# Kernel optimization log

Measured on AMD Instinct MI355X. Metric: run time of the kernel, lower is better.

Reference implementation:

```python
import jax, jax.numpy as jnp
import numpy as np

N_NODES = 20000
N_EDGES = 320000
IN_CH = 512
HID = 128
HEADS = 4
OUT_CH = 30
NEG_SLOPE = 0.2  # PyG GATConv default negative_slope


def add_self_loops(ei, n):
    loops = jnp.arange(n, dtype=ei.dtype)
    return jnp.concatenate([ei, jnp.stack([loops, loops])], axis=1)


def gat_layer(x, ei, W, a_src, a_dst, b, concat):
    # x: [N, F_in], ei: [2, E] (source row 0 -> target row 1), W: [F_in, H*C]
    n = x.shape[0]
    H, C = a_src.shape
    h = (x @ W).reshape(n, H, C)                      # [N, H, C]
    src, dst = ei[0], ei[1]
    al_src = jnp.einsum('nhc,hc->nh', h, a_src)       # [N, H]
    al_dst = jnp.einsum('nhc,hc->nh', h, a_dst)
    e = al_src[src] + al_dst[dst]                     # [E, H]
    e = jnp.where(e > 0, e, NEG_SLOPE * e)            # LeakyReLU
    # segment softmax over destination nodes (stable)
    emax = jax.lax.stop_gradient(jax.ops.segment_max(e, dst, num_segments=n))
    p = jnp.exp(e - emax[dst])
    denom = jax.ops.segment_sum(p, dst, num_segments=n)
    alpha = p / denom[dst]                            # [E, H]
    msg = h[src] * alpha[:, :, None]                  # [E, H, C]
    out = jax.ops.segment_sum(msg, dst, num_segments=n)  # [N, H, C]
    out = out.reshape(n, H * C) if concat else out.mean(axis=1)
    return out + b


def setup_inputs() -> dict:
    key = jax.random.key(0)
    ks = jax.random.split(key, 12)
    s = 0.05
    x = jax.random.normal(ks[0], (N_NODES, IN_CH), jnp.float32)
    edge_index = jax.random.randint(ks[1], (2, N_EDGES), 0, N_NODES, jnp.int32)
    return {
        'x': x,
        'edge_index': edge_index,
        'W1': jax.random.normal(ks[2], (IN_CH, HEADS * HID), jnp.float32) * s,
        'a_src1': jax.random.normal(ks[3], (HEADS, HID), jnp.float32) * s,
        'a_dst1': jax.random.normal(ks[4], (HEADS, HID), jnp.float32) * s,
        'b1': jnp.zeros((HEADS * HID,), jnp.float32),
        'W2': jax.random.normal(ks[5], (HEADS * HID, OUT_CH), jnp.float32) * s,
        'a_src2': jax.random.normal(ks[6], (1, OUT_CH), jnp.float32) * s,
        'a_dst2': jax.random.normal(ks[7], (1, OUT_CH), jnp.float32) * s,
        'b2': jnp.zeros((OUT_CH,), jnp.float32),
        'Wd': jax.random.normal(ks[8], (OUT_CH, IN_CH), jnp.float32) * s,
        'bd': jnp.zeros((IN_CH,), jnp.float32),
    }


def reference(x, edge_index, W1, a_src1, a_dst1, b1, W2, a_src2, a_dst2, b2, Wd, bd):
    n = x.shape[0]
    ei = add_self_loops(edge_index, n)
    h = gat_layer(x, ei, W1, a_src1, a_dst1, b1, concat=True)   # [N, HEADS*HID]
    h = jax.nn.elu(h)                                           # dropout is identity in eval
    z = gat_layer(h, ei, W2, a_src2, a_dst2, b2, concat=False)  # [N, OUT_CH]
    x_hat = z @ Wd + bd                                         # [N, IN_CH]
    return (x_hat, z)
```

## Files before the change

kernel.cpp:

```cpp
#include <hip/hip_runtime.h>
#include <hip/hip_bf16.h>
#include <stdint.h>

#define N_NODES 20000
#define N_EDGES 320000
#define IN_CH 512
#define HID 128
#define HEADS 4
#define HC 512
#define OUT_CH 30
#define NEG_SLOPE 0.2f
#define M_PAD 20096
#define CAST_BLOCKS (M_PAD * IN_CH / 4 / 256)
#define G1_BLOCKS (M_PAD / 128 * 4)
#define EDGE_BLOCKS (N_EDGES / 256)
#define MAXDEG 64

typedef _Float16 half8 __attribute__((ext_vector_type(8)));
typedef _Float16 half4v __attribute__((ext_vector_type(4)));
typedef float f32x4 __attribute__((ext_vector_type(4)));

static __device__ __forceinline__ float lrelu(float e) { return e > 0.f ? e : NEG_SLOPE * e; }

static __device__ __forceinline__ void gload16(const void* gsrc, void* ldst) {
  __builtin_amdgcn_global_load_lds(
      (const __attribute__((address_space(1))) uint32_t*)gsrc,
      (__attribute__((address_space(3))) uint32_t*)ldst,
      16, 0, 0);
}

__global__ __launch_bounds__(256) void k_front(const float* __restrict__ x,
                                               const float* __restrict__ W1,
                                               const float* __restrict__ W2,
                                               _Float16* __restrict__ xh,
                                               _Float16* __restrict__ W1t,
                                               _Float16* __restrict__ w2t,
                                               int* __restrict__ cnt) {
  __shared__ float t[64][65];
  const int b = blockIdx.x;
  const int tid = threadIdx.x;
  if (b < CAST_BLOCKS) {
    int i = b * 256 + tid;
    if (i < N_NODES) cnt[i] = 0;
    int base = i * 4;
    int row = base >> 9;
    half4v o;
    if (row < N_NODES) {
      float4 v = *(const float4*)(x + (size_t)base);
      o[0] = (_Float16)v.x; o[1] = (_Float16)v.y; o[2] = (_Float16)v.z; o[3] = (_Float16)v.w;
    } else {
      o[0] = o[1] = o[2] = o[3] = (_Float16)0.f;
    }
    *(half4v*)(xh + (size_t)base) = o;
  } else if (b < CAST_BLOCKS + 64) {
    const int bb = b - CAST_BLOCKS;
    const int bk = (bb & 7) * 64;
    const int bn = (bb >> 3) * 64;
#pragma unroll
    for (int it = 0; it < 16; it++) {
      int idx = tid + it * 256;
      int r = idx >> 6, c = idx & 63;
      t[r][c] = W1[(size_t)(bk + r) * HC + bn + c];
    }
    __syncthreads();
#pragma unroll
    for (int it = 0; it < 16; it++) {
      int idx = tid + it * 256;
      int rn = idx >> 6, ck = idx & 63;
      W1t[(size_t)(bn + rn) * IN_CH + bk + ck] = (_Float16)t[ck][rn];
    }
  } else {
    int idx = (b - CAST_BLOCKS - 64) * 256 + tid;
    int n = idx >> 9, k = idx & 511;
    w2t[idx] = (n < OUT_CH) ? (_Float16)W2[(size_t)k * OUT_CH + n] : (_Float16)0.f;
  }
}

__global__ __launch_bounds__(256) void k_scatter(const int* __restrict__ src,
                                                 const int* __restrict__ dst,
                                                 int* __restrict__ cnt,
                                                 int* __restrict__ srcs) {
  int e = blockIdx.x * 256 + threadIdx.x;
  int d = dst[e];
  int pos = atomicAdd(&cnt[d], 1);
  if (pos < MAXDEG) srcs[(d << 6) + pos] = src[e];
}

__global__ __launch_bounds__(256) void k_gemm1_mfma(const _Float16* __restrict__ A,
                                                    const _Float16* __restrict__ Bt,
                                                    _Float16* __restrict__ C,
                                                    const float* __restrict__ a_src,
                                                    const float* __restrict__ a_dst,
                                                    float* __restrict__ al_s,
                                                    float* __restrict__ al_d) {
  __shared__ _Float16 smem[128 * 136];
  const int bx = blockIdx.x;
  const int tid = threadIdx.x;
  _Float16* As = smem;
  _Float16* Bs = smem + 128 * 64;
  _Float16* Cs = smem;
  const int lane = tid & 63;
  const int w = tid >> 6;
  const int bm = (bx >> 2) * 128;
  const int head = bx & 3;
  const int bn = head * 128;

  const int lrow = lane >> 3;
  const int schunk = (lane & 7) ^ lrow;

  const int wm = w >> 1, wn = w & 1;
  const int r15 = lane & 15;
  const int q = lane >> 4;
  const int a_row0 = wm * 64 + r15;
  const int b_row0 = wn * 64 + r15;

  f32x4 acc[4][4];
  const f32x4 zero = {0.f, 0.f, 0.f, 0.f};
#pragma unroll
  for (int i = 0; i < 4; i++)
#pragma unroll
    for (int j = 0; j < 4; j++) acc[i][j] = zero;

  for (int kb = 0; kb < 8; kb++) {
    const int kof = kb * 64 + schunk * 8;
#pragma unroll
    for (int t = 0; t < 4; t++) {
      const int row = w * 32 + t * 8;
      gload16(A + (size_t)(bm + row + lrow) * IN_CH + kof, (void*)(As + row * 64));
      gload16(Bt + (size_t)(bn + row + lrow) * IN_CH + kof, (void*)(Bs + row * 64));
    }
    __syncthreads();
#pragma unroll
    for (int s = 0; s < 2; s++) {
      const int cs = ((s * 4 + q) ^ (lane & 7)) * 8;
      half8 af[4], bf[4];
#pragma unroll
      for (int i = 0; i < 4; i++) af[i] = *(const half8*)&As[(a_row0 + i * 16) * 64 + cs];
#pragma unroll
      for (int j = 0; j < 4; j++) bf[j] = *(const half8*)&Bs[(b_row0 + j * 16) * 64 + cs];
#pragma unroll
      for (int i = 0; i < 4; i++)
#pragma unroll
        for (int j = 0; j < 4; j++)
          acc[i][j] = __builtin_amdgcn_mfma_f32_16x16x32_f16(af[i], bf[j], acc[i][j], 0, 0, 0);
    }
    __syncthreads();
  }
#pragma unroll
  for (int i = 0; i < 4; i++)
#pragma unroll
    for (int j = 0; j < 4; j++)
#pragma unroll
      for (int r = 0; r < 4; r++) {
        const int row = wm * 64 + i * 16 + q * 4 + r;
        const int col = wn * 64 + j * 16 + r15;
        Cs[row * 136 + col] = (_Float16)acc[i][j][r];
      }
  __syncthreads();
#pragma unroll
  for (int it = 0; it < 8; it++) {
    int cidx = tid + it * 256;
    int row = cidx >> 4, c16 = cidx & 15;
    int gm = bm + row;
    if (gm < N_NODES)
      *(half8*)(C + (size_t)gm * HC + bn + c16 * 8) = *(const half8*)&Cs[row * 136 + c16 * 8];
  }
  const int row = tid >> 1;
  const int hf = tid & 1;
  const float* asp = a_src + head * HID + hf * 64;
  const float* adp = a_dst + head * HID + hf * 64;
  float s = 0.f, d = 0.f;
#pragma unroll
  for (int j8 = 0; j8 < 8; j8++) {
    half8 cv = *(const half8*)&Cs[row * 136 + hf * 64 + j8 * 8];
    float4 a0 = *(const float4*)(asp + j8 * 8);
    float4 a1 = *(const float4*)(asp + j8 * 8 + 4);
    float4 d0 = *(const float4*)(adp + j8 * 8);
    float4 d1 = *(const float4*)(adp + j8 * 8 + 4);
    float c0 = (float)cv[0], c1 = (float)cv[1], c2 = (float)cv[2], c3 = (float)cv[3];
    float c4 = (float)cv[4], c5 = (float)cv[5], c6 = (float)cv[6], c7 = (float)cv[7];
    s += c0 * a0.x + c1 * a0.y + c2 * a0.z + c3 * a0.w +
         c4 * a1.x + c5 * a1.y + c6 * a1.z + c7 * a1.w;
    d += c0 * d0.x + c1 * d0.y + c2 * d0.z + c3 * d0.w +
         c4 * d1.x + c5 * d1.y + c6 * d1.z + c7 * d1.w;
  }
  s += __shfl_xor(s, 1);
  d += __shfl_xor(d, 1);
  const int gm = bm + row;
  if (hf == 0 && gm < N_NODES) {
    al_s[gm * HEADS + head] = s;
    al_d[gm * HEADS + head] = d;
  }
}

__global__ __launch_bounds__(256) void k_agg1(const _Float16* __restrict__ h,
                                              const float* __restrict__ al_s,
                                              const float* __restrict__ al_d,
                                              const int* __restrict__ cnta,
                                              const int* __restrict__ srcs,
                                              const float* __restrict__ b1,
                                              _Float16* __restrict__ hm) {
  __shared__ __align__(16) int2 s_sp[4][64];
  const int tid = threadIdx.x;
  const int lane = tid & 63;
  const int wv = tid >> 6;
  const int qq = lane >> 4;
  const int l16 = lane & 15;
  const int head = blockIdx.x / 1250;
  const int n = (blockIdx.x % 1250) * 16 + wv * 4 + qq;
  const int cb = head * HID + l16 * 8;

  const float adn = al_d[n * HEADS + head];
  const float pself = __expf(lrelu(al_s[n * HEADS + head] + adn));

  half8 hv = *(const half8*)(h + (size_t)n * HC + cb);
  float acc[8];
  float den = pself;
#pragma unroll
  for (int j = 0; j < 8; j++) acc[j] = pself * (float)hv[j];

  const int beg = n << 6;
  const int cnt = min(cnta[n], MAXDEG);
  int mx = cnt;
  mx = max(mx, __shfl_xor(mx, 16));
  mx = max(mx, __shfl_xor(mx, 32));

  for (int base = 0; base < mx; base += 16) {
    int sreg = n;
    float preg = 0.f;
    if (base + l16 < cnt) {
      sreg = srcs[beg + base + l16];
      preg = __expf(lrelu(al_s[sreg * HEADS + head] + adn));
    }
    s_sp[wv][lane] = make_int2(sreg, __float_as_int(preg));
    __builtin_amdgcn_wave_barrier();
    const int rem = cnt - base;
    const int m4 = rem > 16 ? 16 : ((rem + 3) & ~3);
    for (int k = 0; k < m4; k += 4) {
      int4 w0 = *(const int4*)&s_sp[wv][qq * 16 + k];
      int4 w1 = *(const int4*)&s_sp[wv][qq * 16 + k + 2];
      half8 v0 = *(const half8*)(h + (size_t)w0.x * HC + cb);
      half8 v1 = *(const half8*)(h + (size_t)w0.z * HC + cb);
      half8 v2 = *(const half8*)(h + (size_t)w1.x * HC + cb);
      half8 v3 = *(const half8*)(h + (size_t)w1.z * HC + cb);
      float p0 = __int_as_float(w0.y), p1 = __int_as_float(w0.w);
      float p2 = __int_as_float(w1.y), p3 = __int_as_float(w1.w);
      den += p0 + p1 + p2 + p3;
#pragma unroll
      for (int j = 0; j < 8; j++)
        acc[j] += p0 * (float)v0[j] + p1 * (float)v1[j] +
                  p2 * (float)v2[j] + p3 * (float)v3[j];
    }
    __builtin_amdgcn_wave_barrier();
  }
  const float inv = 1.f / den;
  float4 bb0 = *(const float4*)(b1 + cb);
  float4 bb1 = *(const float4*)(b1 + cb + 4);
  float ob[8] = {bb0.x, bb0.y, bb0.z, bb0.w, bb1.x, bb1.y, bb1.z, bb1.w};
  half8 ov;
#pragma unroll
  for (int j = 0; j < 8; j++) {
    float o = acc[j] * inv + ob[j];
    o = o > 0.f ? o : __expf(o) - 1.f;
    ov[j] = (_Float16)o;
  }
  *(half8*)(hm + (size_t)n * HC + cb) = ov;
}

__global__ __launch_bounds__(256) void k_gemm2_mfma(const _Float16* __restrict__ hm,
                                                    const _Float16* __restrict__ w2t,
                                                    const float* __restrict__ a_s2,
                                                    const float* __restrict__ a_d2,
                                                    float* __restrict__ zpre,
                                                    float* __restrict__ al_s2,
                                                    float* __restrict__ al_d2) {
  __shared__ _Float16 Bs[32 * 520];
  __shared__ _Float16 As[64 * 136];
  const int tid = threadIdx.x;
  const int lane = tid & 63;
  const int w = tid >> 6;
  const int bm = blockIdx.x * 64;
  const int n15 = lane & 15;
  const int q = lane >> 4;

#pragma unroll
  for (int it = 0; it < 8; it++) {
    int idx = (tid + it * 256) * 8;
    int n = idx >> 9, k = idx & 511;
    *(half8*)&Bs[n * 520 + k] = *(const half8*)(w2t + idx);
  }

  f32x4 acc0 = {0.f, 0.f, 0.f, 0.f}, acc1 = {0.f, 0.f, 0.f, 0.f};
  for (int kt = 0; kt < HC; kt += 128) {
#pragma unroll
    for (int p = 0; p < 4; p++) {
      int row = (tid >> 4) + p * 16;
      int kof = (tid & 15) * 8;
      int gm = bm + row;
      half8 v = {};
      if (gm < N_NODES) v = *(const half8*)(hm + (size_t)gm * HC + kt + kof);
      *(half8*)&As[row * 136 + kof] = v;
    }
    __syncthreads();
#pragma unroll
    for (int ks = 0; ks < 128; ks += 32) {
      half8 af = *(const half8*)&As[(w * 16 + n15) * 136 + ks + q * 8];
      half8 b0 = *(const half8*)&Bs[n15 * 520 + kt + ks + q * 8];
      half8 b1 = *(const half8*)&Bs[(16 + n15) * 520 + kt + ks + q * 8];
      acc0 = __builtin_amdgcn_mfma_f32_16x16x32_f16(af, b0, acc0, 0, 0, 0);
      acc1 = __builtin_amdgcn_mfma_f32_16x16x32_f16(af, b1, acc1, 0, 0, 0);
    }
    __syncthreads();
  }
  const float asn0 = (n15 < OUT_CH) ? a_s2[n15] : 0.f;
  const float asn1 = (n15 + 16 < OUT_CH) ? a_s2[n15 + 16] : 0.f;
  const float adn0 = (n15 < OUT_CH) ? a_d2[n15] : 0.f;
  const float adn1 = (n15 + 16 < OUT_CH) ? a_d2[n15 + 16] : 0.f;
#pragma unroll
  for (int r = 0; r < 4; r++) {
    const int gm = bm + w * 16 + q * 4 + r;
    const bool ok = gm < N_NODES;
    if (ok) {
      zpre[(size_t)gm * OUT_CH + n15] = acc0[r];
      if (n15 + 16 < OUT_CH) zpre[(size_t)gm * OUT_CH + n15 + 16] = acc1[r];
    }
    float s = acc0[r] * asn0 + acc1[r] * asn1;
    float d = acc0[r] * adn0 + acc1[r] * adn1;
#pragma unroll
    for (int off = 8; off; off >>= 1) {
      s += __shfl_xor(s, off);
      d += __shfl_xor(d, off);
    }
    if (n15 == 0 && ok) {
      al_s2[gm] = s;
      al_d2[gm] = d;
    }
  }
}

__global__ __launch_bounds__(256) void k_agg2dec(const float* __restrict__ zpre,
                                                 const float* __restrict__ al_s2,
                                                 const float* __restrict__ al_d2,
                                                 const int* __restrict__ cnta,
                                                 const int* __restrict__ srcs,
                                                 const float* __restrict__ b2,
                                                 const float* __restrict__ Wd,
                                                 const float* __restrict__ bd,
                                                 float* __restrict__ zout,
                                                 float* __restrict__ xhat) {
  __shared__ __align__(16) int2 s_sp[4][64];
  __shared__ float zs[8][32];
  const int tid = threadIdx.x;
  const int lane = tid & 63;
  const int wv = tid >> 6;
  const int hh = lane >> 5;
  const int l32 = lane & 31;
  const int n = blockIdx.x * 8 + wv * 2 + hh;
  const float ad2n = al_d2[n];
  const float pself = __expf(lrelu(al_s2[n] + ad2n));
  const bool act = l32 < OUT_CH;
  float zv = act ? zpre[(size_t)n * OUT_CH + l32] : 0.f;
  float acc = pself * zv;
  float den = pself;

  const int beg = n << 6;
  const int cnt = min(cnta[n], MAXDEG);
  int mx = max(cnt, __shfl_xor(cnt, 32));

  for (int base = 0; base < mx; base += 32) {
    int sreg = n;
    float preg = 0.f;
    if (base + l32 < cnt) {
      sreg = srcs[beg + base + l32];
      preg = __expf(lrelu(al_s2[sreg] + ad2n));
    }
    s_sp[wv][lane] = make_int2(sreg, __float_as_int(preg));
    __builtin_amdgcn_wave_barrier();
    const int rem = cnt - base;
    const int m4 = rem > 32 ? 32 : ((rem + 3) & ~3);
    for (int k = 0; k < m4; k += 4) {
      int4 w0 = *(const int4*)&s_sp[wv][hh * 32 + k];
      int4 w1 = *(const int4*)&s_sp[wv][hh * 32 + k + 2];
      float v0 = act ? zpre[(size_t)w0.x * OUT_CH + l32] : 0.f;
      float v1 = act ? zpre[(size_t)w0.z * OUT_CH + l32] : 0.f;
      float v2 = act ? zpre[(size_t)w1.x * OUT_CH + l32] : 0.f;
      float v3 = act ? zpre[(size_t)w1.z * OUT_CH + l32] : 0.f;
      float p0 = __int_as_float(w0.y), p1 = __int_as_float(w0.w);
      float p2 = __int_as_float(w1.y), p3 = __int_as_float(w1.w);
      den += p0 + p1 + p2 + p3;
      acc += p0 * v0 + p1 * v1 + p2 * v2 + p3 * v3;
    }
    __builtin_amdgcn_wave_barrier();
  }
  float zfin = 0.f;
  if (act) zfin = acc / den + b2[l32];
  zs[wv * 2 + hh][l32] = zfin;
  if (act) zout[(size_t)n * OUT_CH + l32] = zfin;
  __syncthreads();
  const int n0 = blockIdx.x * 8;
#pragma unroll
  for (int cc = 0; cc < 2; cc++) {
    const int c = cc * 256 + tid;
    float wd[32];
#pragma unroll
    for (int k = 0; k < OUT_CH; k++) wd[k] = Wd[(size_t)k * IN_CH + c];
    wd[30] = wd[31] = 0.f;
    const float b0 = bd[c];
#pragma unroll
    for (int i = 0; i < 8; i++) {
      float a0 = b0;
#pragma unroll
      for (int k4 = 0; k4 < 8; k4++) {
        float4 z4 = *(const float4*)&zs[i][k4 * 4];
        a0 += z4.x * wd[k4 * 4 + 0] + z4.y * wd[k4 * 4 + 1] +
              z4.z * wd[k4 * 4 + 2] + z4.w * wd[k4 * 4 + 3];
      }
      xhat[(size_t)(n0 + i) * IN_CH + c] = a0;
    }
  }
}

extern "C" void kernel_launch(void* const* d_in, const int* in_sizes, int n_in,
                              void* d_out, int out_size, void* d_ws, size_t ws_size,
                              hipStream_t stream) {
  const float* x    = (const float*)d_in[0];
  const int*   ei   = (const int*)d_in[1];
  const float* W1   = (const float*)d_in[2];
  const float* a_s1 = (const float*)d_in[3];
  const float* a_d1 = (const float*)d_in[4];
  const float* b1   = (const float*)d_in[5];
  const float* W2   = (const float*)d_in[6];
  const float* a_s2 = (const float*)d_in[7];
  const float* a_d2 = (const float*)d_in[8];
  const float* b2   = (const float*)d_in[9];
  const float* Wd   = (const float*)d_in[10];
  const float* bd   = (const float*)d_in[11];

  float* xhat = (float*)d_out;
  float* zout = xhat + (size_t)N_NODES * IN_CH;

  const int* srcv = ei;
  const int* dstv = ei + N_EDGES;

  char* w = (char*)d_ws;
  auto alloc = [&](size_t bytes) {
    void* p = (void*)w;
    w += (bytes + 255) & ~(size_t)255;
    return p;
  };
  _Float16* xh   = (_Float16*)alloc((size_t)M_PAD * IN_CH * 2);
  _Float16* w1t  = (_Float16*)alloc((size_t)HC * IN_CH * 2);
  _Float16* w2t  = (_Float16*)alloc((size_t)32 * HC * 2);
  _Float16* h    = (_Float16*)alloc((size_t)N_NODES * HC * 2);
  _Float16* hm   = (_Float16*)alloc((size_t)N_NODES * HC * 2);
  float* zpre  = (float*)alloc((size_t)N_NODES * OUT_CH * 4);
  float* al_s1v= (float*)alloc((size_t)N_NODES * HEADS * 4);
  float* al_d1v= (float*)alloc((size_t)N_NODES * HEADS * 4);
  float* al_s2v= (float*)alloc((size_t)N_NODES * 4);
  float* al_d2v= (float*)alloc((size_t)N_NODES * 4);
  int*   cnt   = (int*)alloc((size_t)N_NODES * 4);
  int*   srcs  = (int*)alloc((size_t)N_NODES * MAXDEG * 4);

  k_front<<<CAST_BLOCKS + 128, 256, 0, stream>>>(x, W1, W2, xh, w1t, w2t, cnt);
  k_scatter<<<EDGE_BLOCKS, 256, 0, stream>>>(srcv, dstv, cnt, srcs);
  k_gemm1_mfma<<<G1_BLOCKS, 256, 0, stream>>>(xh, w1t, h, a_s1, a_d1, al_s1v, al_d1v);
  k_agg1<<<1250 * HEADS, 256, 0, stream>>>(h, al_s1v, al_d1v, cnt, srcs, b1, hm);
  k_gemm2_mfma<<<(N_NODES + 63) / 64, 256, 0, stream>>>(hm, w2t, a_s2, a_d2, zpre,
                                                        al_s2v, al_d2v);
  k_agg2dec<<<N_NODES / 8, 256, 0, stream>>>(zpre, al_s2v, al_d2v, cnt, srcs, b2,
                                             Wd, bd, zout, xhat);
}
```

Measured before the change: 249.1 us.

## Fold edge scatter into front kernel and split aggregation from decoder GEMM

The edge-bucketing scatter now runs inside the front kernel alongside the casts and weight transposes, so one launch is gone. The count array is cleared by a memset beforehand instead of inside the kernel. The fused layer-2 aggregation and decoder is split into two kernels. The new decoder tile covers 64 nodes per block, which reuses the Wd registers across more rows. The trade-off is an extra launch plus a memset, and the z round-trip through global memory.

```diff
diff --git a/kernel.cpp b/kernel.cpp
--- a/kernel.cpp
+++ b/kernel.cpp
@@ -35,13 +35,23 @@
                                                _Float16* __restrict__ xh,
                                                _Float16* __restrict__ W1t,
                                                _Float16* __restrict__ w2t,
-                                               int* __restrict__ cnt) {
+                                               const int* __restrict__ src,
+                                               const int* __restrict__ dst,
+                                               int* __restrict__ cnt,
+                                               int* __restrict__ srcs) {
   __shared__ float t[64][65];
-  const int b = blockIdx.x;
-  const int tid = threadIdx.x;
+  const int b0 = blockIdx.x;
+  const int tid = threadIdx.x;
+  if (b0 < EDGE_BLOCKS) {
+    int e = b0 * 256 + tid;
+    int d = dst[e];
+    int pos = atomicAdd(&cnt[d], 1);
+    if (pos < MAXDEG) srcs[(d << 6) + pos] = src[e];
+    return;
+  }
+  const int b = b0 - EDGE_BLOCKS;
   if (b < CAST_BLOCKS) {
     int i = b * 256 + tid;
-    if (i < N_NODES) cnt[i] = 0;
     int base = i * 4;
     int row = base >> 9;
     half4v o;
@@ -74,16 +84,6 @@
     int n = idx >> 9, k = idx & 511;
     w2t[idx] = (n < OUT_CH) ? (_Float16)W2[(size_t)k * OUT_CH + n] : (_Float16)0.f;
   }
-}
-
-__global__ __launch_bounds__(256) void k_scatter(const int* __restrict__ src,
-                                                 const int* __restrict__ dst,
-                                                 int* __restrict__ cnt,
-                                                 int* __restrict__ srcs) {
-  int e = blockIdx.x * 256 + threadIdx.x;
-  int d = dst[e];
-  int pos = atomicAdd(&cnt[d], 1);
-  if (pos < MAXDEG) srcs[(d << 6) + pos] = src[e];
 }
 
 __global__ __launch_bounds__(256) void k_gemm1_mfma(const _Float16* __restrict__ A,
@@ -338,18 +338,14 @@
   }
 }
 
-__global__ __launch_bounds__(256) void k_agg2dec(const float* __restrict__ zpre,
-                                                 const float* __restrict__ al_s2,
-                                                 const float* __restrict__ al_d2,
-                                                 const int* __restrict__ cnta,
-                                                 const int* __restrict__ srcs,
-                                                 const float* __restrict__ b2,
-                                                 const float* __restrict__ Wd,
-                                                 const float* __restrict__ bd,
-                                                 float* __restrict__ zout,
-                                                 float* __restrict__ xhat) {
+__global__ __launch_bounds__(256) void k_agg2(const float* __restrict__ zpre,
+                                              const float* __restrict__ al_s2,
+                                              const float* __restrict__ al_d2,
+                                              const int* __restrict__ cnta,
+                                              const int* __restrict__ srcs,
+                                              const float* __restrict__ b2,
+                                              float* __restrict__ zout) {
   __shared__ __align__(16) int2 s_sp[4][64];
-  __shared__ float zs[8][32];
   const int tid = threadIdx.x;
   const int lane = tid & 63;
   const int wv = tid >> 6;
@@ -392,31 +388,39 @@
     }
     __builtin_amdgcn_wave_barrier();
   }
-  float zfin = 0.f;
-  if (act) zfin = acc / den + b2[l32];
-  zs[wv * 2 + hh][l32] = zfin;
-  if (act) zout[(size_t)n * OUT_CH + l32] = zfin;
+  if (act) zout[(size_t)n * OUT_CH + l32] = acc / den + b2[l32];
+}
+
+__global__ __launch_bounds__(256) void k_dec(const float* __restrict__ z,
+                                             const float* __restrict__ Wd,
+                                             const float* __restrict__ bd,
+                                             float* __restrict__ xhat) {
+  __shared__ float zs[64][32];
+  const int tid = threadIdx.x;
+  const int c = blockIdx.y * 256 + tid;
+  float wd[32];
+#pragma unroll
+  for (int k = 0; k < OUT_CH; k++) wd[k] = Wd[(size_t)k * IN_CH + c];
+  wd[30] = wd[31] = 0.f;
+  const int n0 = blockIdx.x * 64;
+  for (int idx = tid; idx < 64 * 32; idx += 256) {
+    int r = idx >> 5, cc = idx & 31;
+    int row = n0 + r;
+    zs[r][cc] = (cc < OUT_CH && row < N_NODES) ? z[(size_t)row * OUT_CH + cc] : 0.f;
+  }
   __syncthreads();
-  const int n0 = blockIdx.x * 8;
-#pragma unroll
-  for (int cc = 0; cc < 2; cc++) {
-    const int c = cc * 256 + tid;
-    float wd[32];
-#pragma unroll
-    for (int k = 0; k < OUT_CH; k++) wd[k] = Wd[(size_t)k * IN_CH + c];
-    wd[30] = wd[31] = 0.f;
-    const float b0 = bd[c];
-#pragma unroll
-    for (int i = 0; i < 8; i++) {
-      float a0 = b0;
-#pragma unroll
-      for (int k4 = 0; k4 < 8; k4++) {
-        float4 z4 = *(const float4*)&zs[i][k4 * 4];
-        a0 += z4.x * wd[k4 * 4 + 0] + z4.y * wd[k4 * 4 + 1] +
-              z4.z * wd[k4 * 4 + 2] + z4.w * wd[k4 * 4 + 3];
-      }
-      xhat[(size_t)(n0 + i) * IN_CH + c] = a0;
-    }
+  const float b0 = bd[c];
+  for (int i = 0; i < 64; i++) {
+    int row = n0 + i;
+    if (row >= N_NODES) break;
+    float a0 = b0;
+#pragma unroll
+    for (int k4 = 0; k4 < 8; k4++) {
+      float4 zv = *(const float4*)&zs[i][k4 * 4];
+      a0 += zv.x * wd[k4 * 4 + 0] + zv.y * wd[k4 * 4 + 1] +
+            zv.z * wd[k4 * 4 + 2] + zv.w * wd[k4 * 4 + 3];
+    }
+    xhat[(size_t)row * IN_CH + c] = a0;
   }
 }
 
@@ -461,12 +465,13 @@
   int*   cnt   = (int*)alloc((size_t)N_NODES * 4);
   int*   srcs  = (int*)alloc((size_t)N_NODES * MAXDEG * 4);
 
-  k_front<<<CAST_BLOCKS + 128, 256, 0, stream>>>(x, W1, W2, xh, w1t, w2t, cnt);
-  k_scatter<<<EDGE_BLOCKS, 256, 0, stream>>>(srcv, dstv, cnt, srcs);
+  hipMemsetAsync(cnt, 0, (size_t)N_NODES * 4, stream);
+  k_front<<<EDGE_BLOCKS + CAST_BLOCKS + 128, 256, 0, stream>>>(x, W1, W2, xh, w1t, w2t,
+                                                               srcv, dstv, cnt, srcs);
   k_gemm1_mfma<<<G1_BLOCKS, 256, 0, stream>>>(xh, w1t, h, a_s1, a_d1, al_s1v, al_d1v);
   k_agg1<<<1250 * HEADS, 256, 0, stream>>>(h, al_s1v, al_d1v, cnt, srcs, b1, hm);
   k_gemm2_mfma<<<(N_NODES + 63) / 64, 256, 0, stream>>>(hm, w2t, a_s2, a_d2, zpre,
                                                         al_s2v, al_d2v);
-  k_agg2dec<<<N_NODES / 8, 256, 0, stream>>>(zpre, al_s2v, al_d2v, cnt, srcs, b2,
-                                             Wd, bd, zout, xhat);
-}
+  k_agg2<<<N_NODES / 8, 256, 0, stream>>>(zpre, al_s2v, al_d2v, cnt, srcs, b2, zout);
+  k_dec<<<dim3((N_NODES + 63) / 64, 2), 256, 0, stream>>>(zout, Wd, bd, xhat);
+}
```

After: 241.7 us. -3.0%, faster.
